# Optimization experiments

Hardware: AMD Instinct MI355X
Metric: run time of the kernel (lower is better)

Reference implementation:

```python
import jax, jax.numpy as jnp
import numpy as np

K = 32          # mc_samples neighbors
CMCO_CI = 16    # penultimate weightnet width
HID = 32        # weightnet hidden width

def swish(x):
    return x * jax.nn.sigmoid(x)

def setup_inputs() -> dict:
    key = jax.random.key(0)
    ks = jax.random.split(key, 12)
    bs, n, d, chin, chout = 8, 4096, 3, 64, 64
    xyz = jax.random.normal(ks[0], (bs, n, d), dtype=jnp.float32)
    vals = jax.random.normal(ks[1], (bs, n, chin), dtype=jnp.float32)
    mask = jnp.ones((bs, n), dtype=bool)
    s = lambda fan_in: 1.0 / np.sqrt(fan_in)
    W1 = jax.random.normal(ks[2], (d, HID), dtype=jnp.float32) * s(d)
    b1 = jnp.zeros((HID,), jnp.float32)
    W2 = jax.random.normal(ks[3], (HID, HID), dtype=jnp.float32) * s(HID)
    b2 = jnp.zeros((HID,), jnp.float32)
    W3 = jax.random.normal(ks[4], (HID, CMCO_CI), dtype=jnp.float32) * s(HID)
    b3 = jnp.zeros((CMCO_CI,), jnp.float32)
    Wl = jax.random.normal(ks[5], (chin * CMCO_CI, chout), dtype=jnp.float32) * s(chin * CMCO_CI)
    bl = jnp.zeros((chout,), jnp.float32)
    return {"xyz": xyz, "vals": vals, "mask": mask,
            "W1": W1, "b1": b1, "W2": W2, "b2": b2, "W3": W3, "b3": b3,
            "Wl": Wl, "bl": bl}

def reference(xyz, vals, mask, W1, b1, W2, b2, W3, b3, Wl, bl):
    bs, n, _ = xyz.shape
    ci = vals.shape[-1]
    # ds_frac == 1 -> query_xyz = xyz, sub_mask = mask (identity subsample)
    # KNN over masked points: squared distances (bs, m, n)
    d2 = (jnp.sum(xyz * xyz, -1)[:, :, None]
          - 2.0 * jnp.einsum('bmd,bnd->bmn', xyz, xyz)
          + jnp.sum(xyz * xyz, -1)[:, None, :])
    d2 = jnp.where(mask[:, None, :], d2, jnp.float32(1e10))
    _, idx = jax.lax.top_k(-d2, K)                       # (bs, m, K) nearest
    gather = jax.vmap(lambda a, i: a[i])                 # per-batch fancy gather
    nbhd_xyz = gather(xyz, idx)                          # (bs, m, K, 3)
    nbhd_vals = gather(vals, idx)                        # (bs, m, K, ci)
    nbhd_mask = gather(mask, idx)                        # (bs, m, K)
    deltas = xyz[:, :, None, :] - nbhd_xyz               # (bs, m, K, 3)
    # WeightNet MLP (swish after every layer, no BN since bn=False)
    h = swish(deltas @ W1 + b1)
    h = swish(h @ W2 + b2)
    w = swish(h @ W3 + b3)                               # (bs, m, K, 16)
    nm = nbhd_mask[..., None]
    w_m = jnp.where(nm, w, 0.0)
    v_m = jnp.where(nm, nbhd_vals, 0.0)
    # masked reduce over neighbors: (bs,m,ci,K) @ (bs,m,K,16) -> (bs,m,ci,16)
    partial = jnp.einsum('bmkc,bmkw->bmcw', v_m, w_m).reshape(bs, n, ci * CMCO_CI)
    out = partial @ Wl + bl                              # (bs, m, chout)
    out = jnp.where(mask[..., None], out, 0.0)
    return out
```

## Files before the change

### kernel.cpp

```cpp
#include <hip/hip_runtime.h>
#include <hip/hip_bf16.h>
#include <stdint.h>

#define N_PTS 4096
#define BSZ   8
#define KNBR  32
#define CI    64
#define CO    64
#define HIDW  32
#define WCI   16
#define CAP   128

typedef __attribute__((ext_vector_type(8))) short bf16x8;
typedef __attribute__((ext_vector_type(4))) float f32x4;
typedef __attribute__((ext_vector_type(2))) float f32x2;

__device__ __forceinline__ unsigned int fkey(float f) {
    unsigned int u = __float_as_uint(f);
    return (u & 0x80000000u) ? ~u : (u | 0x80000000u);
}

__device__ __forceinline__ float swishf(float x) {
    return x / (1.0f + __expf(-x));
}

__device__ __forceinline__ unsigned short f2bf(float f) {
    __hip_bfloat16 h = __float2bfloat16(f);
    return *reinterpret_cast<unsigned short*>(&h);
}

__device__ __forceinline__ unsigned packbf(float lo, float hi) {
    return (unsigned)f2bf(lo) | ((unsigned)f2bf(hi) << 16);
}

__device__ __forceinline__ int keybin(unsigned int k) {
    return (k < 0x80000000u) ? 0 : (int)((k >> 23) & 0xFF);
}
__device__ __forceinline__ int keysub(unsigned int k) {
    return (int)((k >> 15) & 0xFF);
}

__device__ __forceinline__ unsigned int point_key4(const float4* __restrict__ xb4, int p,
                                                   float qx, float qy, float qz, float qn) {
    const float4 P = xb4[p];
    const float dot = __fadd_rn(__fadd_rn(__fmul_rn(qx,P.x), __fmul_rn(qy,P.y)), __fmul_rn(qz,P.z));
    const float d2  = __fadd_rn(__fsub_rn(qn, __fmul_rn(2.0f, dot)), P.w);
    return fkey(d2);
}

__device__ __forceinline__ void hist_select(int c0, int c1, int c2, int c3,
                                            int lane, int KK, int* outB, int* outLo) {
    const int lsum = c0 + c1 + c2 + c3;
    int incl = lsum;
    #pragma unroll
    for (int d = 1; d < 64; d <<= 1) {
        int t = __shfl_up(incl, d);
        if (lane >= d) incl += t;
    }
    const int excl = incl - lsum;
    if (excl < KK && incl >= KK) {
        int run = excl, Bb, lo;
        if (run + c0 >= KK)      { Bb = lane*4+0; lo = run; }
        else { run += c0;
          if (run + c1 >= KK)    { Bb = lane*4+1; lo = run; }
          else { run += c1;
            if (run + c2 >= KK)  { Bb = lane*4+2; lo = run; }
            else { run += c2;      Bb = lane*4+3; lo = run; } } }
        *outB = Bb; *outLo = lo;
    }
}

__global__ void prep_kernel(const float* __restrict__ xyz, const float* __restrict__ Wl,
                            unsigned short* __restrict__ wlr, float4* __restrict__ xyzw)
{
    const int i = blockIdx.x * 256 + threadIdx.x;
    {
        const float* s = xyz + (size_t)i * 3;
        const float x = s[0], y = s[1], z = s[2];
        const float pn = __fadd_rn(__fadd_rn(__fmul_rn(x,x), __fmul_rn(y,y)), __fmul_rn(z,z));
        xyzw[i] = make_float4(x, y, z, pn);
    }
    #pragma unroll
    for (int u = 0; u < 2; ++u) {
        const int f  = i + u * 32768;
        const int b  = f & 7;
        const int L  = (f >> 3) & 63;
        const int kt = (f >> 9) & 31;
        const int nt = f >> 14;
        const int k  = kt * 32 + (L >> 4) * 8 + b;
        const int col = nt * 16 + (L & 15);
        wlr[f] = f2bf(Wl[(size_t)k * CO + col]);
    }
}

__global__ __launch_bounds__(256, 6) void knn_kernel(
    const float4* __restrict__ xyzw, unsigned short* __restrict__ idx_out)
{
    __shared__ alignas(16) unsigned int   hist[4][256][4];
    __shared__ alignas(16) unsigned int   hist2[4][256];
    __shared__ unsigned int   candKey[4][CAP];
    __shared__ unsigned short candIdx[4][CAP];
    __shared__ unsigned short sel[4][KNBR];
    __shared__ int shB[4], shLo[4], shB2[4], shLo2[4];

    const int tid  = threadIdx.x;
    const int lane = tid & 63;
    const int wq   = tid >> 6;
    const int q    = blockIdx.x * 4 + wq;
    const int b    = q >> 12;
    const int m    = q & (N_PTS - 1);

    const float4* xb4 = xyzw + (size_t)b * N_PTS;
    const float4 Q = xb4[m];
    const float qx = Q.x, qy = Q.y, qz = Q.z, qn = Q.w;

    {
        const uint4 z = make_uint4(0u,0u,0u,0u);
        uint4* h1 = reinterpret_cast<uint4*>(&hist[0][0][0]);
        #pragma unroll
        for (int i = 0; i < 4; ++i) h1[tid + i*256] = z;
        uint4* h2 = reinterpret_cast<uint4*>(&hist2[0][0]);
        h2[tid] = z;
    }
    __syncthreads();

    const int sub4 = lane & 3;
    #pragma unroll 4
    for (int s = 0; s < 64; ++s) {
        const unsigned int key = point_key4(xb4, s*64 + lane, qx, qy, qz, qn);
        atomicAdd(&hist[wq][keybin(key)][sub4], 1u);
    }
    __syncthreads();

    {
        const uint4 h0 = *reinterpret_cast<const uint4*>(&hist[wq][lane*4+0][0]);
        const uint4 h1 = *reinterpret_cast<const uint4*>(&hist[wq][lane*4+1][0]);
        const uint4 h2 = *reinterpret_cast<const uint4*>(&hist[wq][lane*4+2][0]);
        const uint4 h3 = *reinterpret_cast<const uint4*>(&hist[wq][lane*4+3][0]);
        hist_select((int)(h0.x+h0.y+h0.z+h0.w), (int)(h1.x+h1.y+h1.z+h1.w),
                    (int)(h2.x+h2.y+h2.z+h2.w), (int)(h3.x+h3.y+h3.z+h3.w),
                    lane, KNBR, &shB[wq], &shLo[wq]);
    }
    __syncthreads();
    const int Bbin = shB[wq];
    const int lo   = shLo[wq];
    const int need = KNBR - lo;

    #pragma unroll 4
    for (int s = 0; s < 64; ++s) {
        const unsigned int key = point_key4(xb4, s*64 + lane, qx, qy, qz, qn);
        if (keybin(key) == Bbin) atomicAdd(&hist2[wq][keysub(key)], 1u);
    }
    __syncthreads();

    {
        const uint4 h = *reinterpret_cast<const uint4*>(&hist2[wq][lane*4]);
        hist_select((int)h.x, (int)h.y, (int)h.z, (int)h.w, lane, need, &shB2[wq], &shLo2[wq]);
    }
    __syncthreads();
    const int B2  = shB2[wq];
    const int lo2 = shLo2[wq];
    const int need3 = need - lo2;

    unsigned long long selMask = 0ull, candMask = 0ull;
    #pragma unroll 4
    for (int s = 0; s < 64; ++s) {
        const unsigned int key = point_key4(xb4, s*64 + lane, qx, qy, qz, qn);
        const int bin = keybin(key);
        bool dsel = (bin < Bbin);
        bool cand = false;
        if (bin == Bbin) {
            const int sb = keysub(key);
            dsel = dsel || (sb < B2);
            cand = (sb == B2);
        }
        if (dsel) selMask  |= (1ull << s);
        if (cand) candMask |= (1ull << s);
    }
    {
        const int combo = __popcll(selMask) | (__popcll(candMask) << 16);
        int incl = combo;
        #pragma unroll
        for (int d = 1; d < 64; d <<= 1) {
            int t = __shfl_up(incl, d);
            if (lane >= d) incl += t;
        }
        const int exclC = incl - combo;
        int pos = exclC & 0xFFFF;
        unsigned long long mm = selMask;
        while (mm) {
            const int s = __builtin_ctzll(mm); mm &= mm - 1ull;
            sel[wq][pos++] = (unsigned short)(s*64 + lane);
        }
        pos = exclC >> 16;
        mm = candMask;
        while (mm) {
            const int s = __builtin_ctzll(mm); mm &= mm - 1ull;
            if (pos < CAP) {
                const int p = s*64 + lane;
                candKey[wq][pos] = point_key4(xb4, p, qx, qy, qz, qn);
                candIdx[wq][pos] = (unsigned short)p;
            }
            ++pos;
        }
        const int totals = __shfl(incl, 63);
        const int candTotal = totals >> 16;
        __syncthreads();

        if (candTotal <= CAP) {
            for (int j = lane; j < candTotal; j += 64) {
                const unsigned long long kkj =
                    ((unsigned long long)candKey[wq][j] << 16) | (unsigned long long)candIdx[wq][j];
                int rank = 0;
                for (int i = 0; i < candTotal; ++i) {
                    const unsigned long long kki =
                        ((unsigned long long)candKey[wq][i] << 16) | (unsigned long long)candIdx[wq][i];
                    rank += (kki < kkj) ? 1 : 0;
                }
                if (rank < need3) sel[wq][lo + lo2 + rank] = candIdx[wq][j];
            }
        } else {
            unsigned long long last = 0ull;
            for (int it = 0; it < need3; ++it) {
                unsigned long long best = ~0ull;
                for (int s = 0; s < 64; ++s) {
                    const int p = s*64 + lane;
                    const unsigned int key = point_key4(xb4, p, qx, qy, qz, qn);
                    if (keybin(key) == Bbin && keysub(key) == B2) {
                        const unsigned long long kk = ((unsigned long long)key << 16) | (unsigned)p;
                        if (kk > last && kk < best) best = kk;
                    }
                }
                #pragma unroll
                for (int off = 32; off; off >>= 1) {
                    const unsigned long long o = __shfl_xor(best, off);
                    if (o < best) best = o;
                }
                last = best;
                if (lane == 0) sel[wq][lo + lo2 + it] = (unsigned short)(best & 0xFFFFull);
            }
        }
    }
    __syncthreads();

    if (lane < KNBR) idx_out[(size_t)q * KNBR + lane] = sel[wq][lane];
}

__global__ __launch_bounds__(512, 2) void fused_kernel(
    const float4* __restrict__ xyzw, const float* __restrict__ vals,
    const unsigned short* __restrict__ knn,
    const float* __restrict__ W1, const float* __restrict__ b1,
    const float* __restrict__ W2, const float* __restrict__ b2,
    const float* __restrict__ W3, const float* __restrict__ b3,
    const unsigned short* __restrict__ wlr, const float* __restrict__ bl,
    float* __restrict__ out)
{
    __shared__ alignas(16) float sW1[96], sb1[32], sW2[1024], sb2[32], sW3[512], sb3[16];
    __shared__ unsigned swv[16][289];
    __shared__ unsigned short ssidx[16][KNBR];
    __shared__ alignas(16) unsigned spartU[16][520];

    const int tid  = threadIdx.x;
    const int lane = tid & 63;
    const int wid  = tid >> 6;

    for (int i = tid; i < 96;   i += 512) sW1[i] = W1[i];
    for (int i = tid; i < 32;   i += 512) sb1[i] = b1[i];
    for (int i = tid; i < 1024; i += 512) sW2[i] = W2[i];
    for (int i = tid; i < 32;   i += 512) sb2[i] = b2[i];
    for (int i = tid; i < 512;  i += 512) sW3[i] = W3[i];
    for (int i = tid; i < 16;   i += 512) sb3[i] = b3[i];
    __syncthreads();

    {
        const int q  = tid >> 5;
        const int k  = tid & 31;
        const int gq = blockIdx.x * 16 + q;
        const int bb = gq >> 12;

        const int nidx = (int)knn[(size_t)gq * KNBR + k];
        ssidx[q][k] = (unsigned short)nidx;
        const float4 Qp = xyzw[gq];
        const float4 Pp = xyzw[(size_t)bb * N_PTS + nidx];
        const float dx = Qp.x - Pp.x;
        const float dy = Qp.y - Pp.y;
        const float dz = Qp.z - Pp.z;

        f32x2 h2a[16];
        #pragma unroll
        for (int j = 0; j < 16; ++j) h2a[j] = *reinterpret_cast<const f32x2*>(&sb2[2*j]);
        #pragma unroll
        for (int i = 0; i < HIDW; ++i) {
            const float h1v = swishf(sb1[i] + dx*sW1[i] + dy*sW1[32+i] + dz*sW1[64+i]);
            #pragma unroll
            for (int j = 0; j < 16; ++j)
                h2a[j] += (*reinterpret_cast<const f32x2*>(&sW2[i*32 + 2*j])) * h1v;
        }
        f32x2 w3a[8];
        #pragma unroll
        for (int j = 0; j < 8; ++j) w3a[j] = *reinterpret_cast<const f32x2*>(&sb3[2*j]);
        #pragma unroll
        for (int i = 0; i < HIDW; ++i) {
            const float hcomp = (i & 1) ? h2a[i >> 1].y : h2a[i >> 1].x;
            const float h2v = swishf(hcomp);
            #pragma unroll
            for (int j = 0; j < 8; ++j)
                w3a[j] += (*reinterpret_cast<const f32x2*>(&sW3[i*16 + 2*j])) * h2v;
        }
        #pragma unroll
        for (int jj = 0; jj < 8; ++jj)
            swv[q][k*9 + jj] = packbf(swishf(w3a[jj].x), swishf(w3a[jj].y));
    }
    __syncthreads();

    {
        const int q2 = tid >> 5;
        const int cp = tid & 31;
        const int c0 = cp * 2;
        const int gq2 = blockIdx.x * 16 + q2;
        const float* vb = vals + ((size_t)(gq2 >> 12)) * N_PTS * CI;

        f32x2 pc0[8], pc1[8];
        #pragma unroll
        for (int j = 0; j < 8; ++j) { pc0[j] = (f32x2){0.f, 0.f}; pc1[j] = (f32x2){0.f, 0.f}; }

        for (int k = 0; k < KNBR; ++k) {
            const int ni = (int)ssidx[q2][k];
            const float2 vv = *reinterpret_cast<const float2*>(vb + (size_t)ni * CI + c0);
            #pragma unroll
            for (int jj = 0; jj < 8; ++jj) {
                const unsigned u = swv[q2][k*9 + jj];
                f32x2 wp;
                wp.x = __uint_as_float(u << 16);
                wp.y = __uint_as_float(u & 0xFFFF0000u);
                pc0[jj] += wp * vv.x;
                pc1[jj] += wp * vv.y;
            }
        }
        #pragma unroll
        for (int jj = 0; jj < 8; ++jj) {
            spartU[q2][c0*8 + jj]     = packbf(pc0[jj].x, pc0[jj].y);
            spartU[q2][(c0+1)*8 + jj] = packbf(pc1[jj].x, pc1[jj].y);
        }
    }
    __syncthreads();

    if (wid < 4) {
        f32x4 acc = {0.f, 0.f, 0.f, 0.f};
        const int nt   = wid;
        const int qrow = lane & 15;
        const int g    = lane >> 4;
        #pragma unroll
        for (int kt = 0; kt < 32; ++kt) {
            const bf16x8 a = *reinterpret_cast<const bf16x8*>(&spartU[qrow][kt*16 + g*4]);
            const bf16x8 bq = *reinterpret_cast<const bf16x8*>(
                wlr + ((size_t)(nt*32 + kt) * 64 + lane) * 8);
            acc = __builtin_amdgcn_mfma_f32_16x16x32_bf16(a, bq, acc, 0, 0, 0);
        }
        const int col = nt*16 + (lane & 15);
        const float blv = bl[col];
        #pragma unroll
        for (int v = 0; v < 4; ++v) {
            const int row = (lane >> 4) * 4 + v;
            const int gq  = blockIdx.x * 16 + row;
            out[(size_t)gq * CO + col] = acc[v] + blv;
        }
    }
}

extern "C" void kernel_launch(void* const* d_in, const int* in_sizes, int n_in,
                              void* d_out, int out_size, void* d_ws, size_t ws_size,
                              hipStream_t stream)
{
    (void)in_sizes; (void)n_in; (void)out_size; (void)ws_size;
    const float* xyz  = (const float*)d_in[0];
    const float* vals = (const float*)d_in[1];
    const float* W1 = (const float*)d_in[3];
    const float* b1 = (const float*)d_in[4];
    const float* W2 = (const float*)d_in[5];
    const float* b2 = (const float*)d_in[6];
    const float* W3 = (const float*)d_in[7];
    const float* b3 = (const float*)d_in[8];
    const float* Wl = (const float*)d_in[9];
    const float* bl = (const float*)d_in[10];
    float* out = (float*)d_out;

    unsigned short* knnbuf = (unsigned short*)d_ws;
    const size_t knnBytes = (size_t)BSZ * N_PTS * KNBR * sizeof(unsigned short);
    unsigned short* wlr = (unsigned short*)((char*)d_ws + knnBytes);
    float4* xyzw = (float4*)((char*)d_ws + knnBytes + 131072);

    prep_kernel<<<dim3(128), dim3(256), 0, stream>>>(xyz, Wl, wlr, xyzw);
    knn_kernel<<<dim3(BSZ * N_PTS / 4), dim3(256), 0, stream>>>(xyzw, knnbuf);
    fused_kernel<<<dim3(BSZ * N_PTS / 16), dim3(512), 0, stream>>>(
        xyzw, vals, knnbuf, W1, b1, W2, b2, W3, b3, wlr, bl, out);
}
```

Baseline: 373.1 us.

## Pack point coords pairwise (SoA float4) to vectorize KNN distance computation

Prep now also writes an interleaved pair layout: one float4 holds x and y for two adjacent points, another holds z and the squared norm. The three KNN histogram and selection passes each load two points per iteration and compute their distances with 2-wide float vector math, so each pass has half as many iterations. Bins are taken straight from the raw float bits instead of an order-preserving key transform, and FP contraction is turned off so results stay bit-exact. This is meant to cut the ALU and load-instruction cost of the distance scans. The price is extra workspace, more prep writes, and remapping the selected bit positions back to point indices.

```diff
diff --git a/kernel.cpp b/kernel.cpp
--- a/kernel.cpp
+++ b/kernel.cpp
@@ -33,19 +33,14 @@
     return (unsigned)f2bf(lo) | ((unsigned)f2bf(hi) << 16);
 }
 
-__device__ __forceinline__ int keybin(unsigned int k) {
-    return (k < 0x80000000u) ? 0 : (int)((k >> 23) & 0xFF);
-}
-__device__ __forceinline__ int keysub(unsigned int k) {
-    return (int)((k >> 15) & 0xFF);
-}
-
-__device__ __forceinline__ unsigned int point_key4(const float4* __restrict__ xb4, int p,
-                                                   float qx, float qy, float qz, float qn) {
-    const float4 P = xb4[p];
-    const float dot = __fadd_rn(__fadd_rn(__fmul_rn(qx,P.x), __fmul_rn(qy,P.y)), __fmul_rn(qz,P.z));
-    const float d2  = __fadd_rn(__fsub_rn(qn, __fmul_rn(2.0f, dot)), P.w);
-    return fkey(d2);
+__device__ __forceinline__ int bin_of(int u) {
+    return (u >= 0x00800000) ? ((u >> 23) & 255) : 0;
+}
+
+__device__ __forceinline__ float d2_exact(float qx, float qy, float qz, float qn,
+                                          float px, float py, float pz, float pw) {
+    const float dot = __fadd_rn(__fadd_rn(__fmul_rn(qx,px), __fmul_rn(qy,py)), __fmul_rn(qz,pz));
+    return __fadd_rn(__fsub_rn(qn, __fmul_rn(2.0f, dot)), pw);
 }
 
 __device__ __forceinline__ void hist_select(int c0, int c1, int c2, int c3,
@@ -71,7 +66,8 @@
 }
 
 __global__ void prep_kernel(const float* __restrict__ xyz, const float* __restrict__ Wl,
-                            unsigned short* __restrict__ wlr, float4* __restrict__ xyzw)
+                            unsigned short* __restrict__ wlr, float4* __restrict__ xyzw,
+                            float4* __restrict__ pxy, float4* __restrict__ pzw)
 {
     const int i = blockIdx.x * 256 + threadIdx.x;
     {
@@ -79,6 +75,11 @@
         const float x = s[0], y = s[1], z = s[2];
         const float pn = __fadd_rn(__fadd_rn(__fmul_rn(x,x), __fmul_rn(y,y)), __fmul_rn(z,z));
         xyzw[i] = make_float4(x, y, z, pn);
+        const int bb = i >> 12, l = i & (N_PTS - 1), pi = l >> 1, h = l & 1;
+        float* XY = (float*)(pxy + (size_t)bb * 2048 + pi);
+        XY[h] = x; XY[2 + h] = y;
+        float* ZW = (float*)(pzw + (size_t)bb * 2048 + pi);
+        ZW[h] = z; ZW[2 + h] = pn;
     }
     #pragma unroll
     for (int u = 0; u < 2; ++u) {
@@ -94,8 +95,10 @@
 }
 
 __global__ __launch_bounds__(256, 6) void knn_kernel(
-    const float4* __restrict__ xyzw, unsigned short* __restrict__ idx_out)
+    const float4* __restrict__ pxy, const float4* __restrict__ pzw,
+    unsigned short* __restrict__ idx_out)
 {
+#pragma clang fp contract(off)
     __shared__ alignas(16) unsigned int   hist[4][256][4];
     __shared__ alignas(16) unsigned int   hist2[4][256];
     __shared__ unsigned int   candKey[4][CAP];
@@ -110,9 +113,16 @@
     const int b    = q >> 12;
     const int m    = q & (N_PTS - 1);
 
-    const float4* xb4 = xyzw + (size_t)b * N_PTS;
-    const float4 Q = xb4[m];
-    const float qx = Q.x, qy = Q.y, qz = Q.z, qn = Q.w;
+    const float4* xy = pxy + (size_t)b * 2048;
+    const float4* zw = pzw + (size_t)b * 2048;
+    const float4 QA = xy[m >> 1];
+    const float4 QB = zw[m >> 1];
+    const int   mh = m & 1;
+    const float qx = mh ? QA.y : QA.x;
+    const float qy = mh ? QA.w : QA.z;
+    const float qz = mh ? QB.y : QB.x;
+    const float qn = mh ? QB.w : QB.z;
+    const f32x2 qn2 = {qn, qn};
 
     {
         const uint4 z = make_uint4(0u,0u,0u,0u);
@@ -125,10 +135,21 @@
     __syncthreads();
 
     const int sub4 = lane & 3;
-    #pragma unroll 4
-    for (int s = 0; s < 64; ++s) {
-        const unsigned int key = point_key4(xb4, s*64 + lane, qx, qy, qz, qn);
-        atomicAdd(&hist[wq][keybin(key)][sub4], 1u);
+    #pragma unroll 2
+    for (int s = 0; s < 32; ++s) {
+        const int pi = s*64 + lane;
+        const f32x4 A = *reinterpret_cast<const f32x4*>(&xy[pi]);
+        const f32x4 Z = *reinterpret_cast<const f32x4*>(&zw[pi]);
+        const f32x2 X2 = __builtin_shufflevector(A, A, 0, 1);
+        const f32x2 Y2 = __builtin_shufflevector(A, A, 2, 3);
+        const f32x2 Z2 = __builtin_shufflevector(Z, Z, 0, 1);
+        const f32x2 W2 = __builtin_shufflevector(Z, Z, 2, 3);
+        const f32x2 dot = (X2*qx + Y2*qy) + Z2*qz;
+        const f32x2 d2  = (qn2 - dot*2.0f) + W2;
+        const int u0 = __float_as_int(d2.x);
+        const int u1 = __float_as_int(d2.y);
+        atomicAdd(&hist[wq][bin_of(u0)][sub4], 1u);
+        atomicAdd(&hist[wq][bin_of(u1)][sub4], 1u);
     }
     __syncthreads();
 
@@ -146,10 +167,21 @@
     const int lo   = shLo[wq];
     const int need = KNBR - lo;
 
-    #pragma unroll 4
-    for (int s = 0; s < 64; ++s) {
-        const unsigned int key = point_key4(xb4, s*64 + lane, qx, qy, qz, qn);
-        if (keybin(key) == Bbin) atomicAdd(&hist2[wq][keysub(key)], 1u);
+    #pragma unroll 2
+    for (int s = 0; s < 32; ++s) {
+        const int pi = s*64 + lane;
+        const f32x4 A = *reinterpret_cast<const f32x4*>(&xy[pi]);
+        const f32x4 Z = *reinterpret_cast<const f32x4*>(&zw[pi]);
+        const f32x2 X2 = __builtin_shufflevector(A, A, 0, 1);
+        const f32x2 Y2 = __builtin_shufflevector(A, A, 2, 3);
+        const f32x2 Z2 = __builtin_shufflevector(Z, Z, 0, 1);
+        const f32x2 W2 = __builtin_shufflevector(Z, Z, 2, 3);
+        const f32x2 dot = (X2*qx + Y2*qy) + Z2*qz;
+        const f32x2 d2  = (qn2 - dot*2.0f) + W2;
+        const int u0 = __float_as_int(d2.x);
+        const int u1 = __float_as_int(d2.y);
+        if (bin_of(u0) == Bbin) atomicAdd(&hist2[wq][(u0 >> 15) & 255], 1u);
+        if (bin_of(u1) == Bbin) atomicAdd(&hist2[wq][(u1 >> 15) & 255], 1u);
     }
     __syncthreads();
 
@@ -163,19 +195,41 @@
     const int need3 = need - lo2;
 
     unsigned long long selMask = 0ull, candMask = 0ull;
-    #pragma unroll 4
-    for (int s = 0; s < 64; ++s) {
-        const unsigned int key = point_key4(xb4, s*64 + lane, qx, qy, qz, qn);
-        const int bin = keybin(key);
-        bool dsel = (bin < Bbin);
-        bool cand = false;
-        if (bin == Bbin) {
-            const int sb = keysub(key);
-            dsel = dsel || (sb < B2);
-            cand = (sb == B2);
-        }
-        if (dsel) selMask  |= (1ull << s);
-        if (cand) candMask |= (1ull << s);
+    #pragma unroll 2
+    for (int s = 0; s < 32; ++s) {
+        const int pi = s*64 + lane;
+        const f32x4 A = *reinterpret_cast<const f32x4*>(&xy[pi]);
+        const f32x4 Z = *reinterpret_cast<const f32x4*>(&zw[pi]);
+        const f32x2 X2 = __builtin_shufflevector(A, A, 0, 1);
+        const f32x2 Y2 = __builtin_shufflevector(A, A, 2, 3);
+        const f32x2 Z2 = __builtin_shufflevector(Z, Z, 0, 1);
+        const f32x2 W2 = __builtin_shufflevector(Z, Z, 2, 3);
+        const f32x2 dot = (X2*qx + Y2*qy) + Z2*qz;
+        const f32x2 d2  = (qn2 - dot*2.0f) + W2;
+        const int u0 = __float_as_int(d2.x);
+        const int u1 = __float_as_int(d2.y);
+        {
+            const int bn = bin_of(u0);
+            bool dsel = (bn < Bbin); bool cand = false;
+            if (bn == Bbin) {
+                const int sb = (u0 >> 15) & 255;
+                dsel = dsel || (sb < B2);
+                cand = (sb == B2);
+            }
+            if (dsel) selMask  |= (1ull << (2*s));
+            if (cand) candMask |= (1ull << (2*s));
+        }
+        {
+            const int bn = bin_of(u1);
+            bool dsel = (bn < Bbin); bool cand = false;
+            if (bn == Bbin) {
+                const int sb = (u1 >> 15) & 255;
+                dsel = dsel || (sb < B2);
+                cand = (sb == B2);
+            }
+            if (dsel) selMask  |= (1ull << (2*s+1));
+            if (cand) candMask |= (1ull << (2*s+1));
+        }
     }
     {
         const int combo = __popcll(selMask) | (__popcll(candMask) << 16);
@@ -189,17 +243,23 @@
         int pos = exclC & 0xFFFF;
         unsigned long long mm = selMask;
         while (mm) {
-            const int s = __builtin_ctzll(mm); mm &= mm - 1ull;
-            sel[wq][pos++] = (unsigned short)(s*64 + lane);
+            const int j = __builtin_ctzll(mm); mm &= mm - 1ull;
+            const int p = 2*((j >> 1)*64 + lane) + (j & 1);
+            sel[wq][pos++] = (unsigned short)p;
         }
         pos = exclC >> 16;
         mm = candMask;
         while (mm) {
-            const int s = __builtin_ctzll(mm); mm &= mm - 1ull;
+            const int j = __builtin_ctzll(mm); mm &= mm - 1ull;
             if (pos < CAP) {
-                const int p = s*64 + lane;
-                candKey[wq][pos] = point_key4(xb4, p, qx, qy, qz, qn);
-                candIdx[wq][pos] = (unsigned short)p;
+                const int pi = (j >> 1)*64 + lane;
+                const int h  = j & 1;
+                const float4 A = xy[pi];
+                const float4 Z = zw[pi];
+                const float px = h ? A.y : A.x, py = h ? A.w : A.z;
+                const float pz = h ? Z.y : Z.x, pw = h ? Z.w : Z.z;
+                candKey[wq][pos] = fkey(d2_exact(qx,qy,qz,qn, px,py,pz,pw));
+                candIdx[wq][pos] = (unsigned short)(2*pi + h);
             }
             ++pos;
         }
@@ -223,12 +283,22 @@
             unsigned long long last = 0ull;
             for (int it = 0; it < need3; ++it) {
                 unsigned long long best = ~0ull;
-                for (int s = 0; s < 64; ++s) {
-                    const int p = s*64 + lane;
-                    const unsigned int key = point_key4(xb4, p, qx, qy, qz, qn);
-                    if (keybin(key) == Bbin && keysub(key) == B2) {
-                        const unsigned long long kk = ((unsigned long long)key << 16) | (unsigned)p;
-                        if (kk > last && kk < best) best = kk;
+                for (int s = 0; s < 32; ++s) {
+                    const int pi = s*64 + lane;
+                    const float4 A = xy[pi];
+                    const float4 Z = zw[pi];
+                    #pragma unroll
+                    for (int h = 0; h < 2; ++h) {
+                        const float px = h ? A.y : A.x, py = h ? A.w : A.z;
+                        const float pz = h ? Z.y : Z.x, pw = h ? Z.w : Z.z;
+                        const float dv = d2_exact(qx,qy,qz,qn, px,py,pz,pw);
+                        const int   uv = __float_as_int(dv);
+                        if (bin_of(uv) == Bbin && ((uv >> 15) & 255) == B2) {
+                            const unsigned key = fkey(dv);
+                            const unsigned long long kk =
+                                ((unsigned long long)key << 16) | (unsigned)(2*pi + h);
+                            if (kk > last && kk < best) best = kk;
+                        }
                     }
                 }
                 #pragma unroll
@@ -385,13 +455,16 @@
     const float* bl = (const float*)d_in[10];
     float* out = (float*)d_out;
 
-    unsigned short* knnbuf = (unsigned short*)d_ws;
+    char* ws = (char*)d_ws;
+    unsigned short* knnbuf = (unsigned short*)ws;
     const size_t knnBytes = (size_t)BSZ * N_PTS * KNBR * sizeof(unsigned short);
-    unsigned short* wlr = (unsigned short*)((char*)d_ws + knnBytes);
-    float4* xyzw = (float4*)((char*)d_ws + knnBytes + 131072);
-
-    prep_kernel<<<dim3(128), dim3(256), 0, stream>>>(xyz, Wl, wlr, xyzw);
-    knn_kernel<<<dim3(BSZ * N_PTS / 4), dim3(256), 0, stream>>>(xyzw, knnbuf);
+    unsigned short* wlr = (unsigned short*)(ws + knnBytes);
+    float4* xyzw = (float4*)(ws + knnBytes + 131072);
+    float4* pxy  = (float4*)(ws + knnBytes + 131072 + 524288);
+    float4* pzw  = (float4*)(ws + knnBytes + 131072 + 524288 + 262144);
+
+    prep_kernel<<<dim3(128), dim3(256), 0, stream>>>(xyz, Wl, wlr, xyzw, pxy, pzw);
+    knn_kernel<<<dim3(BSZ * N_PTS / 4), dim3(256), 0, stream>>>(pxy, pzw, knnbuf);
     fused_kernel<<<dim3(BSZ * N_PTS / 16), dim3(512), 0, stream>>>(
         xyzw, vals, knnbuf, W1, b1, W2, b2, W3, b3, wlr, bl, out);
 }
```

Measured after the change: 329.3 us. 1.13x faster.
